# Kernel optimization log

Measured on AMD Instinct MI355X. Metric: run time of the kernel, lower is better.

## Reference

```python
import jax, jax.numpy as jnp
import numpy as np

N_NODES = 50000
N_EDGES = 800000
D = 128
# PNA avg_deg['log'] from deg histogram: all 50000 nodes have degree 16
# avg_deg_log = sum(log(i+1)*deg[i]) / sum(deg) = log(17)
AVG_DEG_LOG = float(np.log(17.0))
EPS = 1e-5  # PyG StdAggregation epsilon


def setup_inputs() -> dict:
    key = jax.random.key(0)
    k1, k2, k3 = jax.random.split(key, 3)
    x = jax.random.normal(k1, (N_EDGES, D), jnp.float32)
    index = jax.random.randint(k2, (N_EDGES,), 0, N_NODES)
    # nn.Linear(12*D, D): weight [out, in]
    W = jax.random.normal(k3, (D, 12 * D), jnp.float32) * 0.02
    b = jnp.zeros((D,), jnp.float32)
    return {"x": x, "index": index, "W": W, "b": b}


def reference(x, index, W, b):
    N = N_NODES
    ones = jnp.ones((x.shape[0],), x.dtype)
    cnt = jax.ops.segment_sum(ones, index, num_segments=N)          # [N] degree
    cnt_c = jnp.maximum(cnt, 1.0)[:, None]                          # clamp(1)
    s1 = jax.ops.segment_sum(x, index, num_segments=N)              # [N, D]
    s2 = jax.ops.segment_sum(x * x, index, num_segments=N)          # [N, D]
    mean = s1 / cnt_c
    var = s2 / cnt_c - mean * mean
    std = jnp.sqrt(jax.nn.relu(var) + EPS)
    mn = jax.ops.segment_min(x, index, num_segments=N)
    mx = jax.ops.segment_max(x, index, num_segments=N)
    empty = (cnt == 0.0)[:, None]
    mn = jnp.where(empty, 0.0, mn)  # torch_scatter fills empty segments with 0
    mx = jnp.where(empty, 0.0, mx)
    agg = jnp.concatenate([mean, mn, mx, std], axis=-1)             # [N, 4D]
    logd = jnp.log(jnp.maximum(cnt, 1.0) + 1.0)[:, None]
    amp = agg * (logd / AVG_DEG_LOG)                                # amplification
    att = agg * (AVG_DEG_LOG / logd)                                # attenuation
    out = jnp.concatenate([agg, amp, att], axis=-1)                 # [N, 12D]
    return out @ W.T + b                                            # [N, D]
```

## Files before the change

kernel.cpp:

```cpp
#include <hip/hip_runtime.h>
#include <hip/hip_bf16.h>

typedef __attribute__((ext_vector_type(8))) __bf16 bf16x8;
typedef __attribute__((ext_vector_type(4))) float f32x4;

#define AVG_DEG_LOG 2.833213344056216f

__device__ __forceinline__ unsigned short f2bf(float f) {
  union { float f; unsigned int u; } a; a.f = f;
  unsigned int r = a.u + 0x7FFFu + ((a.u >> 16) & 1u);
  return (unsigned short)(r >> 16);
}

__device__ __forceinline__ uint2 pack4(f32x4 a) {
  uint2 u;
  u.x = (unsigned)f2bf(a[0]) | ((unsigned)f2bf(a[1]) << 16);
  u.y = (unsigned)f2bf(a[2]) | ((unsigned)f2bf(a[3]) << 16);
  return u;
}

__global__ void hist_wconv_kernel(const int* __restrict__ idx, int* __restrict__ cnt, int E,
                                  int hb, const float* __restrict__ W,
                                  unsigned short* __restrict__ Wb, int n4) {
  int b = blockIdx.x;
  if (b < hb) {
    int i = b * 256 + threadIdx.x;
    if (i < E) atomicAdd(&cnt[idx[i]], 1);
  } else {
    int i = (b - hb) * 256 + threadIdx.x;
    if (i < n4) {
      float4 v = ((const float4*)W)[i];
      ushort4 o;
      o.x = f2bf(v.x); o.y = f2bf(v.y); o.z = f2bf(v.z); o.w = f2bf(v.w);
      ((ushort4*)Wb)[i] = o;
    }
  }
}

__global__ __launch_bounds__(1024) void scan_kernel(const int* __restrict__ cnt,
                                                    int* __restrict__ offsets, int N) {
  __shared__ int partial[1024];
  int t = threadIdx.x;
  int CH = (N + 1023) >> 10;
  int base = t * CH;
  int s = 0;
  for (int i = 0; i < CH; ++i) { int id = base + i; if (id < N) s += cnt[id]; }
  partial[t] = s;
  __syncthreads();
  int val = s;
  for (int off = 1; off < 1024; off <<= 1) {
    int add = (t >= off) ? partial[t - off] : 0;
    __syncthreads();
    val += add;
    partial[t] = val;
    __syncthreads();
  }
  int run = val - s;
  for (int i = 0; i < CH; ++i) {
    int id = base + i;
    if (id < N) { offsets[id] = run; run += cnt[id]; }
  }
  if (t == 1023) offsets[N] = run;
}

__global__ void scatter_kernel(const int* __restrict__ idx, const int* __restrict__ offsets,
                               int* __restrict__ cursor, int* __restrict__ edge_ids, int E) {
  int i = blockIdx.x * blockDim.x + threadIdx.x;
  if (i < E) {
    int n = idx[i];
    int p = atomicAdd(&cursor[n], 1);
    edge_ids[offsets[n] + p] = i;
  }
}

__global__ __launch_bounds__(256) void agg_kernel(const float* __restrict__ x,
    const int* __restrict__ edge_ids, const int* __restrict__ offsets,
    unsigned short* __restrict__ agg4, float* __restrict__ amp, float* __restrict__ att, int Nn) {
  int wid = blockIdx.x * 4 + (threadIdx.x >> 6);
  if (wid >= Nn) return;
  int lane = threadIdx.x & 63;
  int half = lane >> 5;
  int fh = (lane & 31) * 4;
  int offs = offsets[wid];
  int deg = offsets[wid + 1] - offs;
  f32x4 s = {0.f, 0.f, 0.f, 0.f}, q = {0.f, 0.f, 0.f, 0.f};
  f32x4 mn = {INFINITY, INFINITY, INFINITY, INFINITY};
  f32x4 mx = {-INFINITY, -INFINITY, -INFINITY, -INFINITY};
  const float* xb = x + fh;
  for (int i = 0; i < deg; i += 64) {
    int myid = 0;
    if (i + lane < deg) myid = edge_ids[offs + i + lane];
    int c = deg - i; if (c > 64) c = 64;
    int ii = 0;
    for (; ii + 8 <= c; ii += 8) {
      int e0 = __shfl(myid, ii + half, 64);
      int e1 = __shfl(myid, ii + 2 + half, 64);
      int e2 = __shfl(myid, ii + 4 + half, 64);
      int e3 = __shfl(myid, ii + 6 + half, 64);
      f32x4 v0 = __builtin_nontemporal_load((const f32x4*)(xb + (size_t)e0 * 128));
      f32x4 v1 = __builtin_nontemporal_load((const f32x4*)(xb + (size_t)e1 * 128));
      f32x4 v2 = __builtin_nontemporal_load((const f32x4*)(xb + (size_t)e2 * 128));
      f32x4 v3 = __builtin_nontemporal_load((const f32x4*)(xb + (size_t)e3 * 128));
#pragma unroll
      for (int j = 0; j < 4; ++j) {
        s[j] += v0[j]; q[j] += v0[j] * v0[j]; mn[j] = fminf(mn[j], v0[j]); mx[j] = fmaxf(mx[j], v0[j]);
        s[j] += v1[j]; q[j] += v1[j] * v1[j]; mn[j] = fminf(mn[j], v1[j]); mx[j] = fmaxf(mx[j], v1[j]);
        s[j] += v2[j]; q[j] += v2[j] * v2[j]; mn[j] = fminf(mn[j], v2[j]); mx[j] = fmaxf(mx[j], v2[j]);
        s[j] += v3[j]; q[j] += v3[j] * v3[j]; mn[j] = fminf(mn[j], v3[j]); mx[j] = fmaxf(mx[j], v3[j]);
      }
    }
    for (; ii < c; ii += 2) {
      int p = ii + half;
      bool valid = p < c;
      int e = __shfl(myid, valid ? p : c - 1, 64);
      f32x4 v = __builtin_nontemporal_load((const f32x4*)(xb + (size_t)e * 128));
      if (valid) {
#pragma unroll
        for (int j = 0; j < 4; ++j) {
          s[j] += v[j]; q[j] += v[j] * v[j]; mn[j] = fminf(mn[j], v[j]); mx[j] = fmaxf(mx[j], v[j]);
        }
      }
    }
  }
#pragma unroll
  for (int j = 0; j < 4; ++j) {
    s[j] += __shfl_xor(s[j], 32, 64);
    q[j] += __shfl_xor(q[j], 32, 64);
    mn[j] = fminf(mn[j], __shfl_xor(mn[j], 32, 64));
    mx[j] = fmaxf(mx[j], __shfl_xor(mx[j], 32, 64));
  }
  float cdeg = deg > 0 ? (float)deg : 1.0f;
  float inv = 1.0f / cdeg;
  f32x4 mean, sd;
#pragma unroll
  for (int j = 0; j < 4; ++j) {
    mean[j] = s[j] * inv;
    float var = q[j] * inv - mean[j] * mean[j];
    var = var > 0.f ? var : 0.f;
    sd[j] = sqrtf(var + 1e-5f);
  }
  if (deg == 0) {
#pragma unroll
    for (int j = 0; j < 4; ++j) { mn[j] = 0.f; mx[j] = 0.f; }
  }
  size_t rb = (size_t)wid * 512;
  if (half == 0) {
    *(uint2*)(agg4 + rb + fh)       = pack4(mean);
    *(uint2*)(agg4 + rb + 128 + fh) = pack4(mn);
  } else {
    *(uint2*)(agg4 + rb + 256 + fh) = pack4(mx);
    *(uint2*)(agg4 + rb + 384 + fh) = pack4(sd);
  }
  if (lane == 0) {
    float ld = logf(cdeg + 1.0f);
    amp[wid] = ld / AVG_DEG_LOG;
    att[wid] = AVG_DEG_LOG / ld;
  }
}

__global__ __launch_bounds__(256) void gemm_kernel(
    const unsigned short* __restrict__ agg4, const unsigned short* __restrict__ Wb,
    const float* __restrict__ amp, const float* __restrict__ att,
    const float* __restrict__ bias, float* __restrict__ out, int Nn) {
  __shared__ __align__(16) unsigned short As[64][40];
  __shared__ __align__(16) unsigned short Bs[3][128][40];
  __shared__ float ampS[64], attS[64];
  int t = threadIdx.x;
  int m0 = blockIdx.x * 64;
  if (t < 64) {
    int n = m0 + t; if (n > Nn - 1) n = Nn - 1;
    ampS[t] = amp[n]; attS[t] = att[n];
  }
  int wave = t >> 6, lane = t & 63;
  int arow = lane & 15, quad = lane >> 4;
  f32x4 acc[3][8];
#pragma unroll
  for (int g = 0; g < 3; ++g)
#pragma unroll
    for (int c8 = 0; c8 < 8; ++c8) acc[g][c8] = (f32x4){0.f, 0.f, 0.f, 0.f};

  int ar = t >> 2;
  int akc = (t & 3) * 8;
  int agr = m0 + ar; if (agr > Nn - 1) agr = Nn - 1;
  const unsigned short* aptr = agg4 + (size_t)agr * 512 + akc;

  for (int kk = 0; kk < 512; kk += 32) {
    __syncthreads();
    *(uint4*)&As[ar][akc] = *(const uint4*)(aptr + kk);
#pragma unroll
    for (int j = 0; j < 6; ++j) {
      int idx = t + j * 256;
      int g = idx >> 9;
      int rem = idx & 511;
      int n = rem >> 2;
      int kc = (rem & 3) * 8;
      *(uint4*)&Bs[g][n][kc] = *(const uint4*)(Wb + (size_t)n * 1536 + g * 512 + kk + kc);
    }
    __syncthreads();
    bf16x8 af = *(bf16x8*)&As[wave * 16 + arow][quad * 8];
#pragma unroll
    for (int g = 0; g < 3; ++g) {
#pragma unroll
      for (int c8 = 0; c8 < 8; ++c8) {
        bf16x8 bf = *(bf16x8*)&Bs[g][c8 * 16 + arow][quad * 8];
        acc[g][c8] = __builtin_amdgcn_mfma_f32_16x16x32_bf16(af, bf, acc[g][c8], 0, 0, 0);
      }
    }
  }
#pragma unroll
  for (int c8 = 0; c8 < 8; ++c8) {
    int col = c8 * 16 + arow;
    float bv = bias[col];
#pragma unroll
    for (int r = 0; r < 4; ++r) {
      int lrow = wave * 16 + quad * 4 + r;
      int n = m0 + lrow;
      if (n < Nn) {
        float o = acc[0][c8][r] + ampS[lrow] * acc[1][c8][r] + attS[lrow] * acc[2][c8][r] + bv;
        out[(size_t)n * 128 + col] = o;
      }
    }
  }
}

extern "C" void kernel_launch(void* const* d_in, const int* in_sizes, int n_in,
                              void* d_out, int out_size, void* d_ws, size_t ws_size,
                              hipStream_t stream) {
  const float* x     = (const float*)d_in[0];
  const int*   index = (const int*)d_in[1];
  const float* W     = (const float*)d_in[2];
  const float* bias  = (const float*)d_in[3];
  int E  = in_sizes[1];
  int Nn = out_size / 128;
  float* out = (float*)d_out;

  char* ws = (char*)d_ws;
  size_t off = 0;
  int* cnt     = (int*)(ws + off); off += (size_t)Nn * 4;
  int* cursor  = (int*)(ws + off); off += (size_t)Nn * 4;
  int* offsets = (int*)(ws + off); off += (size_t)(Nn + 1) * 4;
  off = (off + 255) & ~(size_t)255;
  int* edge_ids = (int*)(ws + off); off += (size_t)E * 4;
  off = (off + 255) & ~(size_t)255;
  unsigned short* agg4 = (unsigned short*)(ws + off); off += (size_t)Nn * 512 * 2;
  float* amp = (float*)(ws + off); off += (size_t)Nn * 4;
  float* att = (float*)(ws + off); off += (size_t)Nn * 4;
  off = (off + 255) & ~(size_t)255;
  unsigned short* Wb = (unsigned short*)(ws + off); off += (size_t)128 * 1536 * 2;

  hipMemsetAsync(ws, 0, (size_t)Nn * 8, stream);

  int eb = (E + 255) / 256;
  int n4 = 128 * 1536 / 4;
  int wb = (n4 + 255) / 256;
  hist_wconv_kernel<<<eb + wb, 256, 0, stream>>>(index, cnt, E, eb, W, Wb, n4);
  scan_kernel<<<1, 1024, 0, stream>>>(cnt, offsets, Nn);
  scatter_kernel<<<eb, 256, 0, stream>>>(index, offsets, cursor, edge_ids, E);
  agg_kernel<<<(Nn + 3) / 4, 256, 0, stream>>>(x, edge_ids, offsets, agg4, amp, att, Nn);
  gemm_kernel<<<(Nn + 63) / 64, 256, 0, stream>>>(agg4, Wb, amp, att, bias, out, Nn);
}
```

Before: 751.8 us.

## Fuse all stages into one cooperative persistent kernel with grid syncs

Replaces the five separate launches (histogram plus weight conversion, single-block scan, scatter, aggregation, GEMM) with one cooperative kernel that steps through the stages, separated by grid-wide syncs and grid-stride loops. The prefix scan becomes a distributed two-level scan: a warp-shuffle and block scan, then one block scans the per-block sums. This removes launch gaps and the serial single-block scan. In exchange, the whole kernel carries the GEMM's register and shared-memory footprint, which can lower occupancy in the latency-bound gather phase, and each grid sync adds cost.

```diff
diff --git a/kernel.cpp b/kernel.cpp
--- a/kernel.cpp
+++ b/kernel.cpp
@@ -1,5 +1,8 @@
 #include <hip/hip_runtime.h>
+#include <hip/hip_cooperative_groups.h>
 #include <hip/hip_bf16.h>
+
+namespace cg = cooperative_groups;
 
 typedef __attribute__((ext_vector_type(8))) __bf16 bf16x8;
 typedef __attribute__((ext_vector_type(4))) float f32x4;
@@ -19,205 +22,246 @@
   return u;
 }
 
-__global__ void hist_wconv_kernel(const int* __restrict__ idx, int* __restrict__ cnt, int E,
-                                  int hb, const float* __restrict__ W,
-                                  unsigned short* __restrict__ Wb, int n4) {
-  int b = blockIdx.x;
-  if (b < hb) {
-    int i = b * 256 + threadIdx.x;
-    if (i < E) atomicAdd(&cnt[idx[i]], 1);
-  } else {
-    int i = (b - hb) * 256 + threadIdx.x;
-    if (i < n4) {
-      float4 v = ((const float4*)W)[i];
-      ushort4 o;
-      o.x = f2bf(v.x); o.y = f2bf(v.y); o.z = f2bf(v.z); o.w = f2bf(v.w);
-      ((ushort4*)Wb)[i] = o;
-    }
-  }
-}
-
-__global__ __launch_bounds__(1024) void scan_kernel(const int* __restrict__ cnt,
-                                                    int* __restrict__ offsets, int N) {
-  __shared__ int partial[1024];
-  int t = threadIdx.x;
-  int CH = (N + 1023) >> 10;
-  int base = t * CH;
-  int s = 0;
-  for (int i = 0; i < CH; ++i) { int id = base + i; if (id < N) s += cnt[id]; }
-  partial[t] = s;
-  __syncthreads();
-  int val = s;
-  for (int off = 1; off < 1024; off <<= 1) {
-    int add = (t >= off) ? partial[t - off] : 0;
-    __syncthreads();
-    val += add;
-    partial[t] = val;
-    __syncthreads();
-  }
-  int run = val - s;
-  for (int i = 0; i < CH; ++i) {
-    int id = base + i;
-    if (id < N) { offsets[id] = run; run += cnt[id]; }
-  }
-  if (t == 1023) offsets[N] = run;
-}
-
-__global__ void scatter_kernel(const int* __restrict__ idx, const int* __restrict__ offsets,
-                               int* __restrict__ cursor, int* __restrict__ edge_ids, int E) {
-  int i = blockIdx.x * blockDim.x + threadIdx.x;
-  if (i < E) {
-    int n = idx[i];
-    int p = atomicAdd(&cursor[n], 1);
-    edge_ids[offsets[n] + p] = i;
-  }
-}
-
-__global__ __launch_bounds__(256) void agg_kernel(const float* __restrict__ x,
-    const int* __restrict__ edge_ids, const int* __restrict__ offsets,
-    unsigned short* __restrict__ agg4, float* __restrict__ amp, float* __restrict__ att, int Nn) {
-  int wid = blockIdx.x * 4 + (threadIdx.x >> 6);
-  if (wid >= Nn) return;
-  int lane = threadIdx.x & 63;
-  int half = lane >> 5;
-  int fh = (lane & 31) * 4;
-  int offs = offsets[wid];
-  int deg = offsets[wid + 1] - offs;
-  f32x4 s = {0.f, 0.f, 0.f, 0.f}, q = {0.f, 0.f, 0.f, 0.f};
-  f32x4 mn = {INFINITY, INFINITY, INFINITY, INFINITY};
-  f32x4 mx = {-INFINITY, -INFINITY, -INFINITY, -INFINITY};
-  const float* xb = x + fh;
-  for (int i = 0; i < deg; i += 64) {
-    int myid = 0;
-    if (i + lane < deg) myid = edge_ids[offs + i + lane];
-    int c = deg - i; if (c > 64) c = 64;
-    int ii = 0;
-    for (; ii + 8 <= c; ii += 8) {
-      int e0 = __shfl(myid, ii + half, 64);
-      int e1 = __shfl(myid, ii + 2 + half, 64);
-      int e2 = __shfl(myid, ii + 4 + half, 64);
-      int e3 = __shfl(myid, ii + 6 + half, 64);
-      f32x4 v0 = __builtin_nontemporal_load((const f32x4*)(xb + (size_t)e0 * 128));
-      f32x4 v1 = __builtin_nontemporal_load((const f32x4*)(xb + (size_t)e1 * 128));
-      f32x4 v2 = __builtin_nontemporal_load((const f32x4*)(xb + (size_t)e2 * 128));
-      f32x4 v3 = __builtin_nontemporal_load((const f32x4*)(xb + (size_t)e3 * 128));
-#pragma unroll
-      for (int j = 0; j < 4; ++j) {
-        s[j] += v0[j]; q[j] += v0[j] * v0[j]; mn[j] = fminf(mn[j], v0[j]); mx[j] = fmaxf(mx[j], v0[j]);
-        s[j] += v1[j]; q[j] += v1[j] * v1[j]; mn[j] = fminf(mn[j], v1[j]); mx[j] = fmaxf(mx[j], v1[j]);
-        s[j] += v2[j]; q[j] += v2[j] * v2[j]; mn[j] = fminf(mn[j], v2[j]); mx[j] = fmaxf(mx[j], v2[j]);
-        s[j] += v3[j]; q[j] += v3[j] * v3[j]; mn[j] = fminf(mn[j], v3[j]); mx[j] = fmaxf(mx[j], v3[j]);
-      }
-    }
-    for (; ii < c; ii += 2) {
-      int p = ii + half;
-      bool valid = p < c;
-      int e = __shfl(myid, valid ? p : c - 1, 64);
-      f32x4 v = __builtin_nontemporal_load((const f32x4*)(xb + (size_t)e * 128));
-      if (valid) {
-#pragma unroll
-        for (int j = 0; j < 4; ++j) {
-          s[j] += v[j]; q[j] += v[j] * v[j]; mn[j] = fminf(mn[j], v[j]); mx[j] = fmaxf(mx[j], v[j]);
-        }
-      }
-    }
-  }
-#pragma unroll
-  for (int j = 0; j < 4; ++j) {
-    s[j] += __shfl_xor(s[j], 32, 64);
-    q[j] += __shfl_xor(q[j], 32, 64);
-    mn[j] = fminf(mn[j], __shfl_xor(mn[j], 32, 64));
-    mx[j] = fmaxf(mx[j], __shfl_xor(mx[j], 32, 64));
-  }
-  float cdeg = deg > 0 ? (float)deg : 1.0f;
-  float inv = 1.0f / cdeg;
-  f32x4 mean, sd;
-#pragma unroll
-  for (int j = 0; j < 4; ++j) {
-    mean[j] = s[j] * inv;
-    float var = q[j] * inv - mean[j] * mean[j];
-    var = var > 0.f ? var : 0.f;
-    sd[j] = sqrtf(var + 1e-5f);
-  }
-  if (deg == 0) {
-#pragma unroll
-    for (int j = 0; j < 4; ++j) { mn[j] = 0.f; mx[j] = 0.f; }
-  }
-  size_t rb = (size_t)wid * 512;
-  if (half == 0) {
-    *(uint2*)(agg4 + rb + fh)       = pack4(mean);
-    *(uint2*)(agg4 + rb + 128 + fh) = pack4(mn);
-  } else {
-    *(uint2*)(agg4 + rb + 256 + fh) = pack4(mx);
-    *(uint2*)(agg4 + rb + 384 + fh) = pack4(sd);
-  }
-  if (lane == 0) {
-    float ld = logf(cdeg + 1.0f);
-    amp[wid] = ld / AVG_DEG_LOG;
-    att[wid] = AVG_DEG_LOG / ld;
-  }
-}
-
-__global__ __launch_bounds__(256) void gemm_kernel(
-    const unsigned short* __restrict__ agg4, const unsigned short* __restrict__ Wb,
-    const float* __restrict__ amp, const float* __restrict__ att,
-    const float* __restrict__ bias, float* __restrict__ out, int Nn) {
+__global__ void mega_kernel(
+    const float* __restrict__ x, const int* __restrict__ index,
+    const float* __restrict__ W, const float* __restrict__ bias,
+    int E, int Nn,
+    int* __restrict__ cnt, int* __restrict__ cursor, int* __restrict__ offsets,
+    int* __restrict__ bsums, int* __restrict__ edge_ids,
+    unsigned short* __restrict__ agg4, float* __restrict__ amp, float* __restrict__ att,
+    unsigned short* __restrict__ Wb, float* __restrict__ out) {
+  cg::grid_group grid = cg::this_grid();
   __shared__ __align__(16) unsigned short As[64][40];
   __shared__ __align__(16) unsigned short Bs[3][128][40];
   __shared__ float ampS[64], attS[64];
-  int t = threadIdx.x;
-  int m0 = blockIdx.x * 64;
-  if (t < 64) {
-    int n = m0 + t; if (n > Nn - 1) n = Nn - 1;
-    ampS[t] = amp[n]; attS[t] = att[n];
-  }
-  int wave = t >> 6, lane = t & 63;
-  int arow = lane & 15, quad = lane >> 4;
-  f32x4 acc[3][8];
-#pragma unroll
-  for (int g = 0; g < 3; ++g)
-#pragma unroll
-    for (int c8 = 0; c8 < 8; ++c8) acc[g][c8] = (f32x4){0.f, 0.f, 0.f, 0.f};
-
-  int ar = t >> 2;
-  int akc = (t & 3) * 8;
-  int agr = m0 + ar; if (agr > Nn - 1) agr = Nn - 1;
-  const unsigned short* aptr = agg4 + (size_t)agr * 512 + akc;
-
-  for (int kk = 0; kk < 512; kk += 32) {
+  __shared__ int wsumS[4];
+  __shared__ int tS[256];
+
+  const int t = threadIdx.x;
+  const int lane = t & 63;
+  const int warp = t >> 6;
+  const int G = gridDim.x;
+  const int T = G << 8;
+  const int tid = blockIdx.x * 256 + t;
+
+  const int n4 = 128 * 1536 / 4;
+  for (int i = tid; i < n4; i += T) {
+    float4 v = ((const float4*)W)[i];
+    ushort4 o;
+    o.x = f2bf(v.x); o.y = f2bf(v.y); o.z = f2bf(v.z); o.w = f2bf(v.w);
+    ((ushort4*)Wb)[i] = o;
+  }
+  for (int i = tid; i < E; i += T) atomicAdd(&cnt[index[i]], 1);
+
+  __threadfence();
+  grid.sync();
+
+  int myv = (tid < Nn) ? cnt[tid] : 0;
+  int incl = myv;
+#pragma unroll
+  for (int d = 1; d < 64; d <<= 1) {
+    int u = __shfl_up(incl, d, 64);
+    if (lane >= d) incl += u;
+  }
+  if (lane == 63) wsumS[warp] = incl;
+  __syncthreads();
+  int wpre = 0;
+#pragma unroll
+  for (int w = 0; w < 4; ++w) {
+    int s = wsumS[w];
+    if (w < warp) wpre += s;
+  }
+  if (t == 0) bsums[blockIdx.x] = wsumS[0] + wsumS[1] + wsumS[2] + wsumS[3];
+  __threadfence();
+  grid.sync();
+  if (blockIdx.x == 0) {
+    int K = (G + 255) >> 8;
+    int base = t * K;
+    int vals[8];
+    int s = 0;
+    for (int k = 0; k < K; ++k) {
+      int id = base + k;
+      int v = (id < G) ? bsums[id] : 0;
+      vals[k] = s;
+      s += v;
+    }
+    tS[t] = s;
     __syncthreads();
-    *(uint4*)&As[ar][akc] = *(const uint4*)(aptr + kk);
-#pragma unroll
-    for (int j = 0; j < 6; ++j) {
-      int idx = t + j * 256;
-      int g = idx >> 9;
-      int rem = idx & 511;
-      int n = rem >> 2;
-      int kc = (rem & 3) * 8;
-      *(uint4*)&Bs[g][n][kc] = *(const uint4*)(Wb + (size_t)n * 1536 + g * 512 + kk + kc);
-    }
-    __syncthreads();
-    bf16x8 af = *(bf16x8*)&As[wave * 16 + arow][quad * 8];
-#pragma unroll
-    for (int g = 0; g < 3; ++g) {
+    int val = s;
+    for (int off = 1; off < 256; off <<= 1) {
+      int add = (t >= off) ? tS[t - off] : 0;
+      __syncthreads();
+      val += add;
+      tS[t] = val;
+      __syncthreads();
+    }
+    int excl = val - s;
+    for (int k = 0; k < K; ++k) {
+      int id = base + k;
+      if (id < G) bsums[id] = excl + vals[k];
+    }
+  }
+  __threadfence();
+  grid.sync();
+  int pre = bsums[blockIdx.x] + wpre + (incl - myv);
+  if (tid < Nn) offsets[tid] = pre;
+  if (tid == 0) offsets[Nn] = E;
+
+  __threadfence();
+  grid.sync();
+
+  for (int i = tid; i < E; i += T) {
+    int n = index[i];
+    int p = atomicAdd(&cursor[n], 1);
+    edge_ids[offsets[n] + p] = i;
+  }
+
+  __threadfence();
+  grid.sync();
+
+  {
+    const int nwaves = T >> 6;
+    const int gw = tid >> 6;
+    const int half = lane >> 5;
+    const int fh = (lane & 31) * 4;
+    const float* xb = x + fh;
+    for (int wid = gw; wid < Nn; wid += nwaves) {
+      int offs = offsets[wid];
+      int deg = offsets[wid + 1] - offs;
+      f32x4 s = {0.f, 0.f, 0.f, 0.f}, q = {0.f, 0.f, 0.f, 0.f};
+      f32x4 mn = {INFINITY, INFINITY, INFINITY, INFINITY};
+      f32x4 mx = {-INFINITY, -INFINITY, -INFINITY, -INFINITY};
+      for (int i = 0; i < deg; i += 64) {
+        int myid = 0;
+        if (i + lane < deg) myid = edge_ids[offs + i + lane];
+        int c = deg - i; if (c > 64) c = 64;
+        int ii = 0;
+        for (; ii + 8 <= c; ii += 8) {
+          int e0 = __shfl(myid, ii + half, 64);
+          int e1 = __shfl(myid, ii + 2 + half, 64);
+          int e2 = __shfl(myid, ii + 4 + half, 64);
+          int e3 = __shfl(myid, ii + 6 + half, 64);
+          f32x4 v0 = __builtin_nontemporal_load((const f32x4*)(xb + (size_t)e0 * 128));
+          f32x4 v1 = __builtin_nontemporal_load((const f32x4*)(xb + (size_t)e1 * 128));
+          f32x4 v2 = __builtin_nontemporal_load((const f32x4*)(xb + (size_t)e2 * 128));
+          f32x4 v3 = __builtin_nontemporal_load((const f32x4*)(xb + (size_t)e3 * 128));
+#pragma unroll
+          for (int j = 0; j < 4; ++j) {
+            s[j] += v0[j]; q[j] += v0[j] * v0[j]; mn[j] = fminf(mn[j], v0[j]); mx[j] = fmaxf(mx[j], v0[j]);
+            s[j] += v1[j]; q[j] += v1[j] * v1[j]; mn[j] = fminf(mn[j], v1[j]); mx[j] = fmaxf(mx[j], v1[j]);
+            s[j] += v2[j]; q[j] += v2[j] * v2[j]; mn[j] = fminf(mn[j], v2[j]); mx[j] = fmaxf(mx[j], v2[j]);
+            s[j] += v3[j]; q[j] += v3[j] * v3[j]; mn[j] = fminf(mn[j], v3[j]); mx[j] = fmaxf(mx[j], v3[j]);
+          }
+        }
+        for (; ii < c; ii += 2) {
+          int p = ii + half;
+          bool valid = p < c;
+          int e = __shfl(myid, valid ? p : c - 1, 64);
+          f32x4 v = __builtin_nontemporal_load((const f32x4*)(xb + (size_t)e * 128));
+          if (valid) {
+#pragma unroll
+            for (int j = 0; j < 4; ++j) {
+              s[j] += v[j]; q[j] += v[j] * v[j]; mn[j] = fminf(mn[j], v[j]); mx[j] = fmaxf(mx[j], v[j]);
+            }
+          }
+        }
+      }
+#pragma unroll
+      for (int j = 0; j < 4; ++j) {
+        s[j] += __shfl_xor(s[j], 32, 64);
+        q[j] += __shfl_xor(q[j], 32, 64);
+        mn[j] = fminf(mn[j], __shfl_xor(mn[j], 32, 64));
+        mx[j] = fmaxf(mx[j], __shfl_xor(mx[j], 32, 64));
+      }
+      float cdeg = deg > 0 ? (float)deg : 1.0f;
+      float inv = 1.0f / cdeg;
+      f32x4 mean, sd;
+#pragma unroll
+      for (int j = 0; j < 4; ++j) {
+        mean[j] = s[j] * inv;
+        float var = q[j] * inv - mean[j] * mean[j];
+        var = var > 0.f ? var : 0.f;
+        sd[j] = sqrtf(var + 1e-5f);
+      }
+      if (deg == 0) {
+#pragma unroll
+        for (int j = 0; j < 4; ++j) { mn[j] = 0.f; mx[j] = 0.f; }
+      }
+      size_t rb = (size_t)wid * 512;
+      if (half == 0) {
+        *(uint2*)(agg4 + rb + fh)       = pack4(mean);
+        *(uint2*)(agg4 + rb + 128 + fh) = pack4(mn);
+      } else {
+        *(uint2*)(agg4 + rb + 256 + fh) = pack4(mx);
+        *(uint2*)(agg4 + rb + 384 + fh) = pack4(sd);
+      }
+      if (lane == 0) {
+        float ld = logf(cdeg + 1.0f);
+        amp[wid] = ld / AVG_DEG_LOG;
+        att[wid] = AVG_DEG_LOG / ld;
+      }
+    }
+  }
+
+  __threadfence();
+  grid.sync();
+
+  {
+    const int arow = lane & 15, quad = lane >> 4;
+    const int ar = t >> 2;
+    const int akc = (t & 3) * 8;
+    for (int tile = blockIdx.x; tile * 64 < Nn; tile += G) {
+      int m0 = tile * 64;
+      __syncthreads();
+      if (t < 64) {
+        int n = m0 + t; if (n > Nn - 1) n = Nn - 1;
+        ampS[t] = amp[n]; attS[t] = att[n];
+      }
+      f32x4 acc[3][8];
+#pragma unroll
+      for (int g = 0; g < 3; ++g)
+#pragma unroll
+        for (int c8 = 0; c8 < 8; ++c8) acc[g][c8] = (f32x4){0.f, 0.f, 0.f, 0.f};
+
+      int agr = m0 + ar; if (agr > Nn - 1) agr = Nn - 1;
+      const unsigned short* aptr = agg4 + (size_t)agr * 512 + akc;
+
+      for (int kk = 0; kk < 512; kk += 32) {
+        __syncthreads();
+        *(uint4*)&As[ar][akc] = *(const uint4*)(aptr + kk);
+#pragma unroll
+        for (int j = 0; j < 6; ++j) {
+          int idx = t + j * 256;
+          int g = idx >> 9;
+          int rem = idx & 511;
+          int n = rem >> 2;
+          int kc = (rem & 3) * 8;
+          *(uint4*)&Bs[g][n][kc] = *(const uint4*)(Wb + (size_t)n * 1536 + g * 512 + kk + kc);
+        }
+        __syncthreads();
+        bf16x8 af = *(bf16x8*)&As[warp * 16 + arow][quad * 8];
+#pragma unroll
+        for (int g = 0; g < 3; ++g) {
+#pragma unroll
+          for (int c8 = 0; c8 < 8; ++c8) {
+            bf16x8 bf = *(bf16x8*)&Bs[g][c8 * 16 + arow][quad * 8];
+            acc[g][c8] = __builtin_amdgcn_mfma_f32_16x16x32_bf16(af, bf, acc[g][c8], 0, 0, 0);
+          }
+        }
+      }
 #pragma unroll
       for (int c8 = 0; c8 < 8; ++c8) {
-        bf16x8 bf = *(bf16x8*)&Bs[g][c8 * 16 + arow][quad * 8];
-        acc[g][c8] = __builtin_amdgcn_mfma_f32_16x16x32_bf16(af, bf, acc[g][c8], 0, 0, 0);
-      }
-    }
-  }
-#pragma unroll
-  for (int c8 = 0; c8 < 8; ++c8) {
-    int col = c8 * 16 + arow;
-    float bv = bias[col];
-#pragma unroll
-    for (int r = 0; r < 4; ++r) {
-      int lrow = wave * 16 + quad * 4 + r;
-      int n = m0 + lrow;
-      if (n < Nn) {
-        float o = acc[0][c8][r] + ampS[lrow] * acc[1][c8][r] + attS[lrow] * acc[2][c8][r] + bv;
-        out[(size_t)n * 128 + col] = o;
+        int col = c8 * 16 + arow;
+        float bv = bias[col];
+#pragma unroll
+        for (int r = 0; r < 4; ++r) {
+          int lrow = warp * 16 + quad * 4 + r;
+          int n = m0 + lrow;
+          if (n < Nn) {
+            float o = acc[0][c8][r] + ampS[lrow] * acc[1][c8][r] + attS[lrow] * acc[2][c8][r] + bv;
+            out[(size_t)n * 128 + col] = o;
+          }
+        }
       }
     }
   }
@@ -240,6 +284,7 @@
   int* cursor  = (int*)(ws + off); off += (size_t)Nn * 4;
   int* offsets = (int*)(ws + off); off += (size_t)(Nn + 1) * 4;
   off = (off + 255) & ~(size_t)255;
+  int* bsums   = (int*)(ws + off); off += (size_t)2048 * 4;
   int* edge_ids = (int*)(ws + off); off += (size_t)E * 4;
   off = (off + 255) & ~(size_t)255;
   unsigned short* agg4 = (unsigned short*)(ws + off); off += (size_t)Nn * 512 * 2;
@@ -250,12 +295,19 @@
 
   hipMemsetAsync(ws, 0, (size_t)Nn * 8, stream);
 
-  int eb = (E + 255) / 256;
-  int n4 = 128 * 1536 / 4;
-  int wb = (n4 + 255) / 256;
-  hist_wconv_kernel<<<eb + wb, 256, 0, stream>>>(index, cnt, E, eb, W, Wb, n4);
-  scan_kernel<<<1, 1024, 0, stream>>>(cnt, offsets, Nn);
-  scatter_kernel<<<eb, 256, 0, stream>>>(index, offsets, cursor, edge_ids, E);
-  agg_kernel<<<(Nn + 3) / 4, 256, 0, stream>>>(x, edge_ids, offsets, agg4, amp, att, Nn);
-  gemm_kernel<<<(Nn + 63) / 64, 256, 0, stream>>>(agg4, Wb, amp, att, bias, out, Nn);
+  static int G = 0;
+  if (G == 0) {
+    int mb = 0;
+    hipOccupancyMaxActiveBlocksPerMultiprocessor(&mb, mega_kernel, 256, 0);
+    if (mb < 1) mb = 1;
+    G = mb * 256;
+    if (G > 2048) G = 2048;
+  }
+
+  void* kp[] = {(void*)&x, (void*)&index, (void*)&W, (void*)&bias,
+                (void*)&E, (void*)&Nn,
+                (void*)&cnt, (void*)&cursor, (void*)&offsets, (void*)&bsums,
+                (void*)&edge_ids, (void*)&agg4, (void*)&amp, (void*)&att,
+                (void*)&Wb, (void*)&out};
+  hipLaunchCooperativeKernel((const void*)mega_kernel, dim3(G), dim3(256), kp, 0, stream);
 }
```

New measurement: 1.351 ms. 79.6% more time.
